# Optimization experiments

Measured on AMD Instinct MI355X. Metric: run time of the kernel, lower is better.

Reference implementation:

```python
import jax, jax.numpy as jnp
import numpy as np

B, S, D, H = 4, 2048, 256, 8
HD = D // H  # head_dim = 32
SCALING = HD ** -0.5


def setup_inputs() -> dict:
    key = jax.random.key(0)
    ks = jax.random.split(key, 10)
    glorot = jax.nn.initializers.glorot_uniform()
    inp = {
        "hidden_states": jax.random.normal(ks[0], (B, S, D), jnp.float32),
        "position_embeddings": jax.random.normal(ks[1], (B, S, D), jnp.float32),
        "attention_mask": jnp.zeros((B, S, S), jnp.float32),
        # projection params: EinsumDense 'abc,cde->abde' kernels [D, H, HD]
        "Wq": glorot(ks[2], (D, H, HD), jnp.float32),
        "bq": jnp.zeros((H, HD), jnp.float32),
        "Wk": glorot(ks[3], (D, H, HD), jnp.float32),
        "bk": jnp.zeros((H, HD), jnp.float32),
        "Wv": glorot(ks[4], (D, H, HD), jnp.float32),
        "bv": jnp.zeros((H, HD), jnp.float32),
        # out_proj: 'abc,cd->abd' kernel [D, D]
        "Wo": glorot(ks[5], (D, D), jnp.float32),
        "bo": jnp.zeros((D,), jnp.float32),
    }
    return inp


def reference(hidden_states, position_embeddings, attention_mask,
              Wq, bq, Wk, bk, Wv, bv, Wo, bo):
    # Q/K use hidden + pos embeddings; V uses original hidden states
    hp = hidden_states + position_embeddings
    q = jnp.einsum("bsd,dhe->bshe", hp, Wq) + bq            # [B,S,H,HD]
    k = jnp.einsum("bsd,dhe->bshe", hp, Wk) + bk
    v = jnp.einsum("bsd,dhe->bshe", hidden_states, Wv) + bv
    q = q * SCALING
    scores = jnp.einsum("bqhe,bkhe->bhqk", q, k)            # [B,H,S,S]
    scores = scores + attention_mask[:, None, :, :]         # additive mask
    attn = jax.nn.softmax(scores, axis=-1)
    ctx = jnp.einsum("bhqk,bkhe->bqhe", attn, v)            # [B,S,H,HD]
    ctx = ctx.reshape(ctx.shape[0], ctx.shape[1], D)        # [B,S,D]
    out = jnp.einsum("bsd,de->bse", ctx, Wo) + bo
    return out
```

## Files before the change

kernel.cpp:

```cpp
#include <hip/hip_runtime.h>
#include <hip/hip_bf16.h>

#define Bsz 4
#define Ssz 2048
#define Dsz 256
#define Hh 8
#define HDd 32

typedef __attribute__((ext_vector_type(8))) short bh8;
typedef __attribute__((ext_vector_type(4))) float f4;
typedef __attribute__((ext_vector_type(4))) unsigned u4;
typedef __attribute__((ext_vector_type(2))) unsigned u2;

#define SCAL 0.17677669529663687f
#define LOG2E 1.4426950408889634f
#define QSCALE (SCAL * LOG2E)

__device__ __forceinline__ short f2bf(float f) {
    union { float f; unsigned u; } x; x.f = f;
    unsigned r = x.u + 0x7fffu + ((x.u >> 16) & 1u);
    return (short)(r >> 16);
}

__device__ __forceinline__ float bf2f(short s) {
    union { unsigned u; float f; } x;
    x.u = ((unsigned)(unsigned short)s) << 16;
    return x.f;
}

__device__ __forceinline__ float fexp2(float x) {
#if __has_builtin(__builtin_amdgcn_exp2f)
    return __builtin_amdgcn_exp2f(x);
#else
    float r; asm("v_exp_f32 %0, %1" : "=v"(r) : "v"(x)); return r;
#endif
}

__device__ __forceinline__ unsigned cvtpk(float lo, float hi) {
    unsigned r; asm("v_cvt_pk_bf16_f32 %0, %1, %2" : "=v"(r) : "v"(lo), "v"(hi));
    return r;
}

__device__ __forceinline__ void gload16(const void* g, void* l) {
    __builtin_amdgcn_global_load_lds(
        (const __attribute__((address_space(1))) unsigned int*)g,
        (__attribute__((address_space(3))) unsigned int*)l, 16, 0, 0);
}

__global__ __launch_bounds__(256) void prep_fast(
    const float* __restrict__ hid, const float* __restrict__ pos,
    const float* __restrict__ Wq, const float* __restrict__ Wk,
    const float* __restrict__ Wv, const float* __restrict__ Wo,
    const float* __restrict__ bq,
    short* __restrict__ Wf, float* __restrict__ bqs,
    short* __restrict__ hp, short* __restrict__ hv,
    int* __restrict__ flag)
{
    const int bid = blockIdx.x;
    if (bid < 256) {
        int t = bid * 256 + threadIdx.x;
        int d = t >> 8, n = t & 255;
        int off = (((d >> 5) * 16 + (n >> 4)) * 64 + ((d >> 3) & 3) * 16 + (n & 15)) * 8 + (d & 7);
        Wf[off]          = f2bf(Wq[t] * QSCALE);
        Wf[65536 + off]  = f2bf(Wk[t]);
        Wf[131072 + off] = f2bf(Wv[t]);
        Wf[196608 + off] = f2bf(Wo[t]);
        if (t == 0) *flag = 0;
        if (t < 256) bqs[t] = bq[t] * QSCALE;
    } else {
        const size_t i = ((size_t)(bid - 256) * 256 + threadIdx.x) * 8;
        f4 h1 = *(const f4*)(hid + i), h2 = *(const f4*)(hid + i + 4);
        f4 p1 = *(const f4*)(pos + i), p2 = *(const f4*)(pos + i + 4);
        union { unsigned u[4]; bh8 v; } a, b;
        a.u[0] = cvtpk(h1[0] + p1[0], h1[1] + p1[1]);
        a.u[1] = cvtpk(h1[2] + p1[2], h1[3] + p1[3]);
        a.u[2] = cvtpk(h2[0] + p2[0], h2[1] + p2[1]);
        a.u[3] = cvtpk(h2[2] + p2[2], h2[3] + p2[3]);
        b.u[0] = cvtpk(h1[0], h1[1]); b.u[1] = cvtpk(h1[2], h1[3]);
        b.u[2] = cvtpk(h2[0], h2[1]); b.u[3] = cvtpk(h2[2], h2[3]);
        *(bh8*)(hp + i) = a.v;
        *(bh8*)(hv + i) = b.v;
    }
}

__global__ __launch_bounds__(256) void qkv_scan(
    const short* __restrict__ hp, const short* __restrict__ hv,
    const short* __restrict__ Wf, const float* __restrict__ bqs,
    const float* __restrict__ bk, const float* __restrict__ bv,
    const float* __restrict__ mask, int* __restrict__ flag,
    short* __restrict__ Q, short* __restrict__ K, short* __restrict__ Vt)
{
    const int bid = blockIdx.x;
    if (bid >= 512) {
        const u4* p = (const u4*)mask + (size_t)(bid - 512) * 4096 + threadIdx.x;
        u4 v[16];
#pragma unroll
        for (int k = 0; k < 16; k++) v[k] = p[(size_t)k * 256];
        const unsigned M = 0x7fffffffu;
        u4 o = (v[0] & M) | (v[1] & M);
#pragma unroll
        for (int k = 2; k < 16; k++) o |= (v[k] & M);
        unsigned a = (o[0] | o[1]) | (o[2] | o[3]);
        if (a != 0u) atomicOr(flag, 1);
        return;
    }
    __shared__ __align__(16) char lds[16384];
    const int tid = threadIdx.x;
    const int w = tid >> 6, lane = tid & 63;
    const int lg = lane >> 4, lr = lane & 15;
    const int m0 = bid * 16;
    const int b = m0 >> 11, s0 = m0 & 2047;

    const char* hpg = (const char*)(hp + (size_t)m0 * 256);
    const char* hvg = (const char*)(hv + (size_t)m0 * 256);
    const int rsub = lr * 512 + lg * 16;
#pragma unroll
    for (int i = 0; i < 2; i++) {
        const int k0g = i * 4 + w;
        const int src = k0g * 64 + rsub;
        const int dst = k0g * 1024;
        gload16(hpg + src, lds + dst);
        gload16(hvg + src, lds + 8192 + dst);
    }
    asm volatile("s_waitcnt vmcnt(0)" ::: "memory");
    __builtin_amdgcn_s_barrier();

    const int vhalf = (s0 >> 4) & 1;
#pragma unroll
    for (int ky = 0; ky < 3; ky++) {
        const char* Al = lds + (ky < 2 ? 0 : 8192);
        const short* Wb = Wf + ky * 65536 + (w * 4) * 512 + lane * 8;
        f4 acc[4];
#pragma unroll
        for (int t = 0; t < 4; t++) acc[t] = (f4){0.f, 0.f, 0.f, 0.f};
#pragma unroll
        for (int k0g = 0; k0g < 8; k0g++) {
            bh8 af  = *(const bh8*)(Al + k0g * 1024 + lane * 16);
            bh8 bf0 = *(const bh8*)(Wb + k0g * 8192);
            bh8 bf1 = *(const bh8*)(Wb + k0g * 8192 + 512);
            bh8 bf2 = *(const bh8*)(Wb + k0g * 8192 + 1024);
            bh8 bf3 = *(const bh8*)(Wb + k0g * 8192 + 1536);
            if (ky < 2) {
                acc[0] = __builtin_amdgcn_mfma_f32_16x16x32_bf16(bf0, af, acc[0], 0, 0, 0);
                acc[1] = __builtin_amdgcn_mfma_f32_16x16x32_bf16(bf1, af, acc[1], 0, 0, 0);
                acc[2] = __builtin_amdgcn_mfma_f32_16x16x32_bf16(bf2, af, acc[2], 0, 0, 0);
                acc[3] = __builtin_amdgcn_mfma_f32_16x16x32_bf16(bf3, af, acc[3], 0, 0, 0);
            } else {
                acc[0] = __builtin_amdgcn_mfma_f32_16x16x32_bf16(af, bf0, acc[0], 0, 0, 0);
                acc[1] = __builtin_amdgcn_mfma_f32_16x16x32_bf16(af, bf1, acc[1], 0, 0, 0);
                acc[2] = __builtin_amdgcn_mfma_f32_16x16x32_bf16(af, bf2, acc[2], 0, 0, 0);
                acc[3] = __builtin_amdgcn_mfma_f32_16x16x32_bf16(af, bf3, acc[3], 0, 0, 0);
            }
        }
        if (ky < 2) {
            short* P = (ky == 0) ? Q : K;
            const float* bb = (ky == 0) ? bqs : bk;
            const int s = s0 + lr;
#pragma unroll
            for (int nt = 0; nt < 4; nt++) {
                const int nb = w * 64 + nt * 16 + lg * 4;
                const int h = nb >> 5, hd = nb & 31;
                f4 bias = *(const f4*)(bb + nb);
                u2 o = { cvtpk(acc[nt][0] + bias[0], acc[nt][1] + bias[1]),
                         cvtpk(acc[nt][2] + bias[2], acc[nt][3] + bias[3]) };
                *(u2*)(P + ((size_t)(b * Hh + h) * Ssz + s) * HDd + hd) = o;
            }
        } else {
#pragma unroll
            for (int nt = 0; nt < 4; nt++) {
                const int n = w * 64 + nt * 16 + lr;
                const int h = n >> 5, hd = n & 31;
                const float bias = bv[n];
                u2 o = { cvtpk(acc[nt][0] + bias, acc[nt][1] + bias),
                         cvtpk(acc[nt][2] + bias, acc[nt][3] + bias) };
                *(u2*)(Vt + ((size_t)(b * Hh + h) * HDd + hd) * Ssz
                           + (s0 & ~31) + lg * 8 + vhalf * 4) = o;
            }
        }
    }
}

template<int NS>
__global__ __launch_bounds__(512) void attn(
    const short* __restrict__ Q, const short* __restrict__ Kb,
    const short* __restrict__ Vt, const float* __restrict__ mask,
    const int* __restrict__ flag, short* __restrict__ ctx,
    short* __restrict__ pacc, float* __restrict__ sums)
{
    __shared__ __align__(16) char lds[24576];
    const int tid = threadIdx.x;
    const int bh = blockIdx.y, b = bh >> 3, h = bh & 7;
    const int w = tid >> 6, lane = tid & 63;
    const int lg = lane >> 4, lr = lane & 15;
    const int q0 = blockIdx.x * 128 + w * 16;
    const int kz0 = blockIdx.z * (Ssz / NS);
    constexpr int NT = Ssz / NS / 64;

    const char* Kg = (const char*)(Kb + (size_t)bh * Ssz * HDd);
    const char* Vg = (const char*)(Vt + (size_t)bh * HDd * Ssz);
    const bool um = (*flag) != 0;
    const float* mrow = mask + ((size_t)b * Ssz + q0 + lr) * Ssz;

    const char* sgp;
    size_t sstep;
    int ldo;
    if (w < 4) {
        const int kt = w * 64 + lane;
        const int kx = (kt * 16) ^ (((kt >> 3) & 3) << 4);
        sgp = Kg + (size_t)kz0 * 64 + kx;
        sstep = 4096;
        ldo = w * 1024;
    } else {
        const int vt2 = (w - 4) * 64 + lane;
        const int vrow = vt2 >> 3;
        const int vcol = ((vt2 & 7) * 16) ^ ((vrow & 7) << 4);
        sgp = Vg + (size_t)vrow * (Ssz * 2) + (size_t)kz0 * 2 + vcol;
        sstep = 128;
        ldo = 4096 + (w - 4) * 1024;
    }

    const int koff  = (lr * 64 + lg * 16) ^ (((lr >> 1) & 3) << 4);
    const int voff0 = 4096 + ((lr * 128 + lg * 16) ^ ((lr & 7) << 4));
    const int voff1 = voff0 ^ 64;

    bh8 qf = *(const bh8*)(Q + ((size_t)bh * Ssz + q0 + lr) * HDd + lg * 8);
    const f4 c8 = {-8.f, -8.f, -8.f, -8.f};
    f4 acc0 = {0.f, 0.f, 0.f, 0.f}, acc1 = {0.f, 0.f, 0.f, 0.f};
    f4 sm = {0.f, 0.f, 0.f, 0.f};
    union { unsigned u[4]; bh8 v; } ones;
#pragma unroll
    for (int j = 0; j < 4; j++) ones.u[j] = 0x3F803F80u;

    auto stage = [&](int t, int buf) {
        gload16(sgp + (size_t)t * sstep, lds + buf * 8192 + ldo);
    };

    auto compute = [&](int t, int bs) {
        const char* kp = lds + bs + koff;
        bh8 k0 = *(const bh8*)(kp);
        bh8 k1 = *(const bh8*)(kp + 1024);
        bh8 k2 = *(const bh8*)(kp + 2048);
        bh8 k3 = *(const bh8*)(kp + 3072);
        const char* vp = lds + bs;
        bh8 v00 = *(const bh8*)(vp + voff0);
        bh8 v01 = *(const bh8*)(vp + voff1);
        bh8 v10 = *(const bh8*)(vp + voff0 + 2048);
        bh8 v11 = *(const bh8*)(vp + voff1 + 2048);

        __builtin_amdgcn_s_setprio(1);
        f4 s0 = __builtin_amdgcn_mfma_f32_16x16x32_bf16(k0, qf, c8, 0, 0, 0);
        f4 s1 = __builtin_amdgcn_mfma_f32_16x16x32_bf16(k1, qf, c8, 0, 0, 0);
        f4 s2 = __builtin_amdgcn_mfma_f32_16x16x32_bf16(k2, qf, c8, 0, 0, 0);
        f4 s3 = __builtin_amdgcn_mfma_f32_16x16x32_bf16(k3, qf, c8, 0, 0, 0);
        __builtin_amdgcn_s_setprio(0);
        if (um) {
            const int kb = kz0 + t * 64;
            f4 m0v = *(const f4*)(mrow + kb + lg * 4);
            f4 m1v = *(const f4*)(mrow + kb + 16 + lg * 4);
            f4 m2v = *(const f4*)(mrow + kb + 32 + lg * 4);
            f4 m3v = *(const f4*)(mrow + kb + 48 + lg * 4);
            s0 += m0v * LOG2E; s1 += m1v * LOG2E; s2 += m2v * LOG2E; s3 += m3v * LOG2E;
        }

        float p[16];
#pragma unroll
        for (int j = 0; j < 4; j++) {
            p[j]      = fexp2(s0[j]);
            p[4 + j]  = fexp2(s1[j]);
            p[8 + j]  = fexp2(s2[j]);
            p[12 + j] = fexp2(s3[j]);
        }
        union { unsigned u[4]; bh8 v; } pf0, pf1;
        pf0.u[0] = cvtpk(p[0], p[1]);   pf0.u[1] = cvtpk(p[2], p[3]);
        pf0.u[2] = cvtpk(p[4], p[5]);   pf0.u[3] = cvtpk(p[6], p[7]);
        pf1.u[0] = cvtpk(p[8], p[9]);   pf1.u[1] = cvtpk(p[10], p[11]);
        pf1.u[2] = cvtpk(p[12], p[13]); pf1.u[3] = cvtpk(p[14], p[15]);

        __builtin_amdgcn_s_setprio(1);
        acc0 = __builtin_amdgcn_mfma_f32_16x16x32_bf16(v00, pf0.v, acc0, 0, 0, 0);
        acc0 = __builtin_amdgcn_mfma_f32_16x16x32_bf16(v01, pf1.v, acc0, 0, 0, 0);
        acc1 = __builtin_amdgcn_mfma_f32_16x16x32_bf16(v10, pf0.v, acc1, 0, 0, 0);
        acc1 = __builtin_amdgcn_mfma_f32_16x16x32_bf16(v11, pf1.v, acc1, 0, 0, 0);
        sm   = __builtin_amdgcn_mfma_f32_16x16x32_bf16(ones.v, pf0.v, sm, 0, 0, 0);
        sm   = __builtin_amdgcn_mfma_f32_16x16x32_bf16(ones.v, pf1.v, sm, 0, 0, 0);
        __builtin_amdgcn_s_setprio(0);
    };

    stage(0, 0);
    stage(1, 1);
    for (int t = 0; t < NT - 1; ++t) {
        asm volatile("s_waitcnt vmcnt(1)" ::: "memory");
        __builtin_amdgcn_s_barrier();
        if (t + 2 < NT) stage(t + 2, (t + 2) % 3);
        compute(t, (t % 3) * 8192);
    }
    asm volatile("s_waitcnt vmcnt(0)" ::: "memory");
    __builtin_amdgcn_s_barrier();
    compute(NT - 1, ((NT - 1) % 3) * 8192);

    const float sum = sm[0];

    if constexpr (NS == 1) {
        float inv = 1.f / sum;
        short* cp = ctx + ((size_t)(b * Ssz + q0 + lr)) * Dsz + h * HDd + lg * 4;
#pragma unroll
        for (int r = 0; r < 4; r++) {
            cp[r]      = f2bf(acc0[r] * inv);
            cp[16 + r] = f2bf(acc1[r] * inv);
        }
    } else {
        const size_t rbase = ((size_t)blockIdx.z * (Bsz * Hh) + bh) * Ssz + q0 + lr;
        short* pa = pacc + rbase * HDd;
        *(u2*)(pa + lg * 4)      = (u2){cvtpk(acc0[0], acc0[1]), cvtpk(acc0[2], acc0[3])};
        *(u2*)(pa + 16 + lg * 4) = (u2){cvtpk(acc1[0], acc1[1]), cvtpk(acc1[2], acc1[3])};
        if (lg == 0) sums[rbase] = sum;
    }
}

template<int SPLIT>
__global__ __launch_bounds__(256) void out_gemm(
    const short* __restrict__ ctx, const short* __restrict__ pacc,
    const float* __restrict__ sums, const short* __restrict__ WfO,
    const float* __restrict__ bo, float* __restrict__ out)
{
    const int w = threadIdx.x >> 6, lane = threadIdx.x & 63;
    const int lg = lane >> 4, lr = lane & 15;
    const int m0 = blockIdx.x * 16;
    const int row = m0 + lr;
    const int b = row >> 11, q = row & 2047;
    f4 acc[4];
#pragma unroll
    for (int t = 0; t < 4; t++) acc[t] = (f4){0.f, 0.f, 0.f, 0.f};
    const short* ap = ctx + (size_t)row * 256 + lg * 8;
    const short* Wb = WfO + (w * 4) * 512 + lane * 8;
    constexpr size_t R = (size_t)(Bsz * Hh) * Ssz;
#pragma unroll
    for (int k0g = 0; k0g < 8; k0g++) {
        union { unsigned u[4]; bh8 v; } af;
        if constexpr (SPLIT) {
            const int h = k0g;
            const size_t pr = ((size_t)(b * Hh + h)) * Ssz + q;
            const float inv = 1.f / (sums[pr] + sums[R + pr]);
            bh8 x0 = *(const bh8*)(pacc + pr * HDd + lg * 8);
            bh8 x1 = *(const bh8*)(pacc + (R + pr) * HDd + lg * 8);
            af.u[0] = cvtpk((bf2f(x0[0]) + bf2f(x1[0])) * inv, (bf2f(x0[1]) + bf2f(x1[1])) * inv);
            af.u[1] = cvtpk((bf2f(x0[2]) + bf2f(x1[2])) * inv, (bf2f(x0[3]) + bf2f(x1[3])) * inv);
            af.u[2] = cvtpk((bf2f(x0[4]) + bf2f(x1[4])) * inv, (bf2f(x0[5]) + bf2f(x1[5])) * inv);
            af.u[3] = cvtpk((bf2f(x0[6]) + bf2f(x1[6])) * inv, (bf2f(x0[7]) + bf2f(x1[7])) * inv);
        } else {
            af.v = *(const bh8*)(ap + k0g * 32);
        }
#pragma unroll
        for (int nt = 0; nt < 4; nt++) {
            bh8 bf = *(const bh8*)(Wb + k0g * 8192 + nt * 512);
            acc[nt] = __builtin_amdgcn_mfma_f32_16x16x32_bf16(bf, af.v, acc[nt], 0, 0, 0);
        }
    }
#pragma unroll
    for (int nt = 0; nt < 4; nt++) {
        const int nb = w * 64 + nt * 16 + lg * 4;
        f4 bias = *(const f4*)(bo + nb);
        f4 res = acc[nt] + bias;
        *(f4*)(out + (size_t)row * 256 + nb) = res;
    }
}

extern "C" void kernel_launch(void* const* d_in, const int* in_sizes, int n_in,
                              void* d_out, int out_size, void* d_ws, size_t ws_size,
                              hipStream_t stream)
{
    const float* hid  = (const float*)d_in[0];
    const float* pos  = (const float*)d_in[1];
    const float* mask = (const float*)d_in[2];
    const float* Wq   = (const float*)d_in[3];
    const float* bq   = (const float*)d_in[4];
    const float* Wk   = (const float*)d_in[5];
    const float* bk   = (const float*)d_in[6];
    const float* Wv   = (const float*)d_in[7];
    const float* bv   = (const float*)d_in[8];
    const float* Wo   = (const float*)d_in[9];
    const float* bo   = (const float*)d_in[10];
    float* out = (float*)d_out;

    char* ws = (char*)d_ws;
    short* Wf   = (short*)(ws);
    float* bqs  = (float*)(ws + (512 << 10));
    int*   flag = (int*)  (ws + (516 << 10));
    short* hp   = (short*)(ws + (1  << 20));
    short* hv   = (short*)(ws + (5  << 20));
    short* Qb   = (short*)(ws + (9  << 20));
    short* Kb   = (short*)(ws + (13 << 20));
    short* Vtb  = (short*)(ws + (17 << 20));
    short* ctxb = (short*)(ws + (21 << 20));
    short* pacc = (short*)(ws + (25 << 20));
    float* sums = (float*)(ws + (34 << 20));

    prep_fast<<<1280, 256, 0, stream>>>(hid, pos, Wq, Wk, Wv, Wo, bq, Wf, bqs, hp, hv, flag);
    qkv_scan<<<1536, 256, 0, stream>>>(hp, hv, Wf, bqs, bk, bv, mask, flag, Qb, Kb, Vtb);

    const bool split = ws_size >= ((size_t)36 << 20);
    if (split) {
        attn<2><<<dim3(16, 32, 2), 512, 0, stream>>>(Qb, Kb, Vtb, mask, flag, ctxb, pacc, sums);
        out_gemm<1><<<512, 256, 0, stream>>>(ctxb, pacc, sums, Wf + 196608, bo, out);
    } else {
        attn<1><<<dim3(16, 32, 1), 512, 0, stream>>>(Qb, Kb, Vtb, mask, flag, ctxb, pacc, sums);
        out_gemm<0><<<512, 256, 0, stream>>>(ctxb, pacc, sums, Wf + 196608, bo, out);
    }
}
```

Baseline: 65.91 us.

## Double query rows per attention wave and fuse input conversion into QKV projection

The attention kernel now has each wave process 32 query rows instead of 16, so every K/V fragment loaded from LDS feeds twice as many MFMAs. The grid is halved to match and the launch bounds gain an occupancy hint. Separately, the fp32-to-bf16 conversion of hidden+pos and hidden is moved out of the prep kernel into the QKV kernel's LDS staging, which removes the intermediate hp/hv round trip through global memory. In exchange, attention uses more registers per wave and runs fewer blocks, and the QKV kernel now waits on synchronous fp32 global loads.

New measurement: 64.39 us. -2.3%, faster.

```diff
diff --git a/kernel.cpp b/kernel.cpp
--- a/kernel.cpp
+++ b/kernel.cpp
@@ -48,43 +48,25 @@
 }
 
 __global__ __launch_bounds__(256) void prep_fast(
-    const float* __restrict__ hid, const float* __restrict__ pos,
     const float* __restrict__ Wq, const float* __restrict__ Wk,
     const float* __restrict__ Wv, const float* __restrict__ Wo,
     const float* __restrict__ bq,
     short* __restrict__ Wf, float* __restrict__ bqs,
-    short* __restrict__ hp, short* __restrict__ hv,
     int* __restrict__ flag)
 {
-    const int bid = blockIdx.x;
-    if (bid < 256) {
-        int t = bid * 256 + threadIdx.x;
-        int d = t >> 8, n = t & 255;
-        int off = (((d >> 5) * 16 + (n >> 4)) * 64 + ((d >> 3) & 3) * 16 + (n & 15)) * 8 + (d & 7);
-        Wf[off]          = f2bf(Wq[t] * QSCALE);
-        Wf[65536 + off]  = f2bf(Wk[t]);
-        Wf[131072 + off] = f2bf(Wv[t]);
-        Wf[196608 + off] = f2bf(Wo[t]);
-        if (t == 0) *flag = 0;
-        if (t < 256) bqs[t] = bq[t] * QSCALE;
-    } else {
-        const size_t i = ((size_t)(bid - 256) * 256 + threadIdx.x) * 8;
-        f4 h1 = *(const f4*)(hid + i), h2 = *(const f4*)(hid + i + 4);
-        f4 p1 = *(const f4*)(pos + i), p2 = *(const f4*)(pos + i + 4);
-        union { unsigned u[4]; bh8 v; } a, b;
-        a.u[0] = cvtpk(h1[0] + p1[0], h1[1] + p1[1]);
-        a.u[1] = cvtpk(h1[2] + p1[2], h1[3] + p1[3]);
-        a.u[2] = cvtpk(h2[0] + p2[0], h2[1] + p2[1]);
-        a.u[3] = cvtpk(h2[2] + p2[2], h2[3] + p2[3]);
-        b.u[0] = cvtpk(h1[0], h1[1]); b.u[1] = cvtpk(h1[2], h1[3]);
-        b.u[2] = cvtpk(h2[0], h2[1]); b.u[3] = cvtpk(h2[2], h2[3]);
-        *(bh8*)(hp + i) = a.v;
-        *(bh8*)(hv + i) = b.v;
-    }
+    int t = blockIdx.x * 256 + threadIdx.x;
+    int d = t >> 8, n = t & 255;
+    int off = (((d >> 5) * 16 + (n >> 4)) * 64 + ((d >> 3) & 3) * 16 + (n & 15)) * 8 + (d & 7);
+    Wf[off]          = f2bf(Wq[t] * QSCALE);
+    Wf[65536 + off]  = f2bf(Wk[t]);
+    Wf[131072 + off] = f2bf(Wv[t]);
+    Wf[196608 + off] = f2bf(Wo[t]);
+    if (t == 0) *flag = 0;
+    if (t < 256) bqs[t] = bq[t] * QSCALE;
 }
 
 __global__ __launch_bounds__(256) void qkv_scan(
-    const short* __restrict__ hp, const short* __restrict__ hv,
+    const float* __restrict__ hid, const float* __restrict__ pos,
     const short* __restrict__ Wf, const float* __restrict__ bqs,
     const float* __restrict__ bk, const float* __restrict__ bv,
     const float* __restrict__ mask, int* __restrict__ flag,
@@ -111,18 +93,28 @@
     const int m0 = bid * 16;
     const int b = m0 >> 11, s0 = m0 & 2047;
 
-    const char* hpg = (const char*)(hp + (size_t)m0 * 256);
-    const char* hvg = (const char*)(hv + (size_t)m0 * 256);
-    const int rsub = lr * 512 + lg * 16;
-#pragma unroll
-    for (int i = 0; i < 2; i++) {
-        const int k0g = i * 4 + w;
-        const int src = k0g * 64 + rsub;
-        const int dst = k0g * 1024;
-        gload16(hpg + src, lds + dst);
-        gload16(hvg + src, lds + 8192 + dst);
-    }
-    asm volatile("s_waitcnt vmcnt(0)" ::: "memory");
+    {
+        const int row = tid >> 4, c = tid & 15;
+        const float* hb = hid + (size_t)(m0 + row) * 256 + c * 16;
+        const float* pb = pos + (size_t)(m0 + row) * 256 + c * 16;
+        f4 h0 = *(const f4*)(hb), h1 = *(const f4*)(hb + 4);
+        f4 h2 = *(const f4*)(hb + 8), h3 = *(const f4*)(hb + 12);
+        f4 p0 = *(const f4*)(pb), p1 = *(const f4*)(pb + 4);
+        f4 p2 = *(const f4*)(pb + 8), p3 = *(const f4*)(pb + 12);
+        const int off = ((c >> 1) * 1024) + (((2 * c) & 3) * 256) + row * 16;
+        u4 hp0 = { cvtpk(h0[0] + p0[0], h0[1] + p0[1]), cvtpk(h0[2] + p0[2], h0[3] + p0[3]),
+                   cvtpk(h1[0] + p1[0], h1[1] + p1[1]), cvtpk(h1[2] + p1[2], h1[3] + p1[3]) };
+        u4 hp1 = { cvtpk(h2[0] + p2[0], h2[1] + p2[1]), cvtpk(h2[2] + p2[2], h2[3] + p2[3]),
+                   cvtpk(h3[0] + p3[0], h3[1] + p3[1]), cvtpk(h3[2] + p3[2], h3[3] + p3[3]) };
+        u4 hv0 = { cvtpk(h0[0], h0[1]), cvtpk(h0[2], h0[3]),
+                   cvtpk(h1[0], h1[1]), cvtpk(h1[2], h1[3]) };
+        u4 hv1 = { cvtpk(h2[0], h2[1]), cvtpk(h2[2], h2[3]),
+                   cvtpk(h3[0], h3[1]), cvtpk(h3[2], h3[3]) };
+        *(u4*)(lds + off)          = hp0;
+        *(u4*)(lds + off + 256)    = hp1;
+        *(u4*)(lds + 8192 + off)       = hv0;
+        *(u4*)(lds + 8192 + off + 256) = hv1;
+    }
     __builtin_amdgcn_s_barrier();
 
     const int vhalf = (s0 >> 4) & 1;
@@ -181,7 +173,7 @@
 }
 
 template<int NS>
-__global__ __launch_bounds__(512) void attn(
+__global__ __launch_bounds__(512, 4) void attn(
     const short* __restrict__ Q, const short* __restrict__ Kb,
     const short* __restrict__ Vt, const float* __restrict__ mask,
     const int* __restrict__ flag, short* __restrict__ ctx,
@@ -192,14 +184,15 @@
     const int bh = blockIdx.y, b = bh >> 3, h = bh & 7;
     const int w = tid >> 6, lane = tid & 63;
     const int lg = lane >> 4, lr = lane & 15;
-    const int q0 = blockIdx.x * 128 + w * 16;
+    const int q0 = blockIdx.x * 256 + w * 32;
     const int kz0 = blockIdx.z * (Ssz / NS);
     constexpr int NT = Ssz / NS / 64;
 
     const char* Kg = (const char*)(Kb + (size_t)bh * Ssz * HDd);
     const char* Vg = (const char*)(Vt + (size_t)bh * HDd * Ssz);
     const bool um = (*flag) != 0;
-    const float* mrow = mask + ((size_t)b * Ssz + q0 + lr) * Ssz;
+    const float* mrow0 = mask + ((size_t)b * Ssz + q0 + lr) * Ssz;
+    const float* mrow1 = mrow0 + (size_t)16 * Ssz;
 
     const char* sgp;
     size_t sstep;
@@ -223,10 +216,12 @@
     const int voff0 = 4096 + ((lr * 128 + lg * 16) ^ ((lr & 7) << 4));
     const int voff1 = voff0 ^ 64;
 
-    bh8 qf = *(const bh8*)(Q + ((size_t)bh * Ssz + q0 + lr) * HDd + lg * 8);
+    const short* Qw = Q + ((size_t)bh * Ssz + q0) * HDd;
+    bh8 qf0 = *(const bh8*)(Qw + (size_t)lr * HDd + lg * 8);
+    bh8 qf1 = *(const bh8*)(Qw + (size_t)(16 + lr) * HDd + lg * 8);
     const f4 c8 = {-8.f, -8.f, -8.f, -8.f};
-    f4 acc0 = {0.f, 0.f, 0.f, 0.f}, acc1 = {0.f, 0.f, 0.f, 0.f};
-    f4 sm = {0.f, 0.f, 0.f, 0.f};
+    f4 a00 = {0.f,0.f,0.f,0.f}, a01 = a00, a10 = a00, a11 = a00;
+    f4 sm0 = a00, sm1 = a00;
     union { unsigned u[4]; bh8 v; } ones;
 #pragma unroll
     for (int j = 0; j < 4; j++) ones.u[j] = 0x3F803F80u;
@@ -248,41 +243,66 @@
         bh8 v11 = *(const bh8*)(vp + voff1 + 2048);
 
         __builtin_amdgcn_s_setprio(1);
-        f4 s0 = __builtin_amdgcn_mfma_f32_16x16x32_bf16(k0, qf, c8, 0, 0, 0);
-        f4 s1 = __builtin_amdgcn_mfma_f32_16x16x32_bf16(k1, qf, c8, 0, 0, 0);
-        f4 s2 = __builtin_amdgcn_mfma_f32_16x16x32_bf16(k2, qf, c8, 0, 0, 0);
-        f4 s3 = __builtin_amdgcn_mfma_f32_16x16x32_bf16(k3, qf, c8, 0, 0, 0);
+        f4 s00 = __builtin_amdgcn_mfma_f32_16x16x32_bf16(k0, qf0, c8, 0, 0, 0);
+        f4 s01 = __builtin_amdgcn_mfma_f32_16x16x32_bf16(k1, qf0, c8, 0, 0, 0);
+        f4 s02 = __builtin_amdgcn_mfma_f32_16x16x32_bf16(k2, qf0, c8, 0, 0, 0);
+        f4 s03 = __builtin_amdgcn_mfma_f32_16x16x32_bf16(k3, qf0, c8, 0, 0, 0);
+        f4 s10 = __builtin_amdgcn_mfma_f32_16x16x32_bf16(k0, qf1, c8, 0, 0, 0);
+        f4 s11 = __builtin_amdgcn_mfma_f32_16x16x32_bf16(k1, qf1, c8, 0, 0, 0);
+        f4 s12 = __builtin_amdgcn_mfma_f32_16x16x32_bf16(k2, qf1, c8, 0, 0, 0);
+        f4 s13 = __builtin_amdgcn_mfma_f32_16x16x32_bf16(k3, qf1, c8, 0, 0, 0);
         __builtin_amdgcn_s_setprio(0);
         if (um) {
             const int kb = kz0 + t * 64;
-            f4 m0v = *(const f4*)(mrow + kb + lg * 4);
-            f4 m1v = *(const f4*)(mrow + kb + 16 + lg * 4);
-            f4 m2v = *(const f4*)(mrow + kb + 32 + lg * 4);
-            f4 m3v = *(const f4*)(mrow + kb + 48 + lg * 4);
-            s0 += m0v * LOG2E; s1 += m1v * LOG2E; s2 += m2v * LOG2E; s3 += m3v * LOG2E;
-        }
-
-        float p[16];
-#pragma unroll
-        for (int j = 0; j < 4; j++) {
-            p[j]      = fexp2(s0[j]);
-            p[4 + j]  = fexp2(s1[j]);
-            p[8 + j]  = fexp2(s2[j]);
-            p[12 + j] = fexp2(s3[j]);
-        }
-        union { unsigned u[4]; bh8 v; } pf0, pf1;
-        pf0.u[0] = cvtpk(p[0], p[1]);   pf0.u[1] = cvtpk(p[2], p[3]);
-        pf0.u[2] = cvtpk(p[4], p[5]);   pf0.u[3] = cvtpk(p[6], p[7]);
-        pf1.u[0] = cvtpk(p[8], p[9]);   pf1.u[1] = cvtpk(p[10], p[11]);
-        pf1.u[2] = cvtpk(p[12], p[13]); pf1.u[3] = cvtpk(p[14], p[15]);
+            s00 += *(const f4*)(mrow0 + kb + lg * 4) * LOG2E;
+            s01 += *(const f4*)(mrow0 + kb + 16 + lg * 4) * LOG2E;
+            s02 += *(const f4*)(mrow0 + kb + 32 + lg * 4) * LOG2E;
+            s03 += *(const f4*)(mrow0 + kb + 48 + lg * 4) * LOG2E;
+            s10 += *(const f4*)(mrow1 + kb + lg * 4) * LOG2E;
+            s11 += *(const f4*)(mrow1 + kb + 16 + lg * 4) * LOG2E;
+            s12 += *(const f4*)(mrow1 + kb + 32 + lg * 4) * LOG2E;
+            s13 += *(const f4*)(mrow1 + kb + 48 + lg * 4) * LOG2E;
+        }
+
+        union { unsigned u[4]; bh8 v; } pf00, pf01, pf10, pf11;
+        {
+            float p[16];
+#pragma unroll
+            for (int j = 0; j < 4; j++) {
+                p[j] = fexp2(s00[j]); p[4+j] = fexp2(s01[j]);
+                p[8+j] = fexp2(s02[j]); p[12+j] = fexp2(s03[j]);
+            }
+            pf00.u[0] = cvtpk(p[0], p[1]);   pf00.u[1] = cvtpk(p[2], p[3]);
+            pf00.u[2] = cvtpk(p[4], p[5]);   pf00.u[3] = cvtpk(p[6], p[7]);
+            pf01.u[0] = cvtpk(p[8], p[9]);   pf01.u[1] = cvtpk(p[10], p[11]);
+            pf01.u[2] = cvtpk(p[12], p[13]); pf01.u[3] = cvtpk(p[14], p[15]);
+        }
+        {
+            float p[16];
+#pragma unroll
+            for (int j = 0; j < 4; j++) {
+                p[j] = fexp2(s10[j]); p[4+j] = fexp2(s11[j]);
+                p[8+j] = fexp2(s12[j]); p[12+j] = fexp2(s13[j]);
+            }
+            pf10.u[0] = cvtpk(p[0], p[1]);   pf10.u[1] = cvtpk(p[2], p[3]);
+            pf10.u[2] = cvtpk(p[4], p[5]);   pf10.u[3] = cvtpk(p[6], p[7]);
+            pf11.u[0] = cvtpk(p[8], p[9]);   pf11.u[1] = cvtpk(p[10], p[11]);
+            pf11.u[2] = cvtpk(p[12], p[13]); pf11.u[3] = cvtpk(p[14], p[15]);
+        }
 
         __builtin_amdgcn_s_setprio(1);
-        acc0 = __builtin_amdgcn_mfma_f32_16x16x32_bf16(v00, pf0.v, acc0, 0, 0, 0);
-        acc0 = __builtin_amdgcn_mfma_f32_16x16x32_bf16(v01, pf1.v, acc0, 0, 0, 0);
-        acc1 = __builtin_amdgcn_mfma_f32_16x16x32_bf16(v10, pf0.v, acc1, 0, 0, 0);
-        acc1 = __builtin_amdgcn_mfma_f32_16x16x32_bf16(v11, pf1.v, acc1, 0, 0, 0);
-        sm   = __builtin_amdgcn_mfma_f32_16x16x32_bf16(ones.v, pf0.v, sm, 0, 0, 0);
-        sm   = __builtin_amdgcn_mfma_f32_16x16x32_bf16(ones.v, pf1.v, sm, 0, 0, 0);
+        a00 = __builtin_amdgcn_mfma_f32_16x16x32_bf16(v00, pf00.v, a00, 0, 0, 0);
+        a00 = __builtin_amdgcn_mfma_f32_16x16x32_bf16(v01, pf01.v, a00, 0, 0, 0);
+        a01 = __builtin_amdgcn_mfma_f32_16x16x32_bf16(v10, pf00.v, a01, 0, 0, 0);
+        a01 = __builtin_amdgcn_mfma_f32_16x16x32_bf16(v11, pf01.v, a01, 0, 0, 0);
+        sm0 = __builtin_amdgcn_mfma_f32_16x16x32_bf16(ones.v, pf00.v, sm0, 0, 0, 0);
+        sm0 = __builtin_amdgcn_mfma_f32_16x16x32_bf16(ones.v, pf01.v, sm0, 0, 0, 0);
+        a10 = __builtin_amdgcn_mfma_f32_16x16x32_bf16(v00, pf10.v, a10, 0, 0, 0);
+        a10 = __builtin_amdgcn_mfma_f32_16x16x32_bf16(v01, pf11.v, a10, 0, 0, 0);
+        a11 = __builtin_amdgcn_mfma_f32_16x16x32_bf16(v10, pf10.v, a11, 0, 0, 0);
+        a11 = __builtin_amdgcn_mfma_f32_16x16x32_bf16(v11, pf11.v, a11, 0, 0, 0);
+        sm1 = __builtin_amdgcn_mfma_f32_16x16x32_bf16(ones.v, pf10.v, sm1, 0, 0, 0);
+        sm1 = __builtin_amdgcn_mfma_f32_16x16x32_bf16(ones.v, pf11.v, sm1, 0, 0, 0);
         __builtin_amdgcn_s_setprio(0);
     };
 
@@ -298,22 +318,31 @@
     __builtin_amdgcn_s_barrier();
     compute(NT - 1, ((NT - 1) % 3) * 8192);
 
-    const float sum = sm[0];
+    const float sum0 = sm0[0], sum1 = sm1[0];
 
     if constexpr (NS == 1) {
-        float inv = 1.f / sum;
-        short* cp = ctx + ((size_t)(b * Ssz + q0 + lr)) * Dsz + h * HDd + lg * 4;
+        float inv0 = 1.f / sum0, inv1 = 1.f / sum1;
+        short* cp0 = ctx + ((size_t)(b * Ssz + q0 + lr)) * Dsz + h * HDd + lg * 4;
+        short* cp1 = cp0 + (size_t)16 * Dsz;
 #pragma unroll
         for (int r = 0; r < 4; r++) {
-            cp[r]      = f2bf(acc0[r] * inv);
-            cp[16 + r] = f2bf(acc1[r] * inv);
+            cp0[r]      = f2bf(a00[r] * inv0);
+            cp0[16 + r] = f2bf(a01[r] * inv0);
+            cp1[r]      = f2bf(a10[r] * inv1);
+            cp1[16 + r] = f2bf(a11[r] * inv1);
         }
     } else {
         const size_t rbase = ((size_t)blockIdx.z * (Bsz * Hh) + bh) * Ssz + q0 + lr;
-        short* pa = pacc + rbase * HDd;
-        *(u2*)(pa + lg * 4)      = (u2){cvtpk(acc0[0], acc0[1]), cvtpk(acc0[2], acc0[3])};
-        *(u2*)(pa + 16 + lg * 4) = (u2){cvtpk(acc1[0], acc1[1]), cvtpk(acc1[2], acc1[3])};
-        if (lg == 0) sums[rbase] = sum;
+        short* pa0 = pacc + rbase * HDd;
+        short* pa1 = pa0 + (size_t)16 * HDd;
+        *(u2*)(pa0 + lg * 4)      = (u2){cvtpk(a00[0], a00[1]), cvtpk(a00[2], a00[3])};
+        *(u2*)(pa0 + 16 + lg * 4) = (u2){cvtpk(a01[0], a01[1]), cvtpk(a01[2], a01[3])};
+        *(u2*)(pa1 + lg * 4)      = (u2){cvtpk(a10[0], a10[1]), cvtpk(a10[2], a10[3])};
+        *(u2*)(pa1 + 16 + lg * 4) = (u2){cvtpk(a11[0], a11[1]), cvtpk(a11[2], a11[3])};
+        if (lg == 0) {
+            sums[rbase]      = sum0;
+            sums[rbase + 16] = sum1;
+        }
     }
 }
 
@@ -386,8 +415,6 @@
     short* Wf   = (short*)(ws);
     float* bqs  = (float*)(ws + (512 << 10));
     int*   flag = (int*)  (ws + (516 << 10));
-    short* hp   = (short*)(ws + (1  << 20));
-    short* hv   = (short*)(ws + (5  << 20));
     short* Qb   = (short*)(ws + (9  << 20));
     short* Kb   = (short*)(ws + (13 << 20));
     short* Vtb  = (short*)(ws + (17 << 20));
@@ -395,15 +422,15 @@
     short* pacc = (short*)(ws + (25 << 20));
     float* sums = (float*)(ws + (34 << 20));
 
-    prep_fast<<<1280, 256, 0, stream>>>(hid, pos, Wq, Wk, Wv, Wo, bq, Wf, bqs, hp, hv, flag);
-    qkv_scan<<<1536, 256, 0, stream>>>(hp, hv, Wf, bqs, bk, bv, mask, flag, Qb, Kb, Vtb);
+    prep_fast<<<256, 256, 0, stream>>>(Wq, Wk, Wv, Wo, bq, Wf, bqs, flag);
+    qkv_scan<<<1536, 256, 0, stream>>>(hid, pos, Wf, bqs, bk, bv, mask, flag, Qb, Kb, Vtb);
 
     const bool split = ws_size >= ((size_t)36 << 20);
     if (split) {
-        attn<2><<<dim3(16, 32, 2), 512, 0, stream>>>(Qb, Kb, Vtb, mask, flag, ctxb, pacc, sums);
+        attn<2><<<dim3(8, 32, 2), 512, 0, stream>>>(Qb, Kb, Vtb, mask, flag, ctxb, pacc, sums);
         out_gemm<1><<<512, 256, 0, stream>>>(ctxb, pacc, sums, Wf + 196608, bo, out);
     } else {
-        attn<1><<<dim3(16, 32, 1), 512, 0, stream>>>(Qb, Kb, Vtb, mask, flag, ctxb, pacc, sums);
+        attn<1><<<dim3(8, 32, 1), 512, 0, stream>>>(Qb, Kb, Vtb, mask, flag, ctxb, pacc, sums);
         out_gemm<0><<<512, 256, 0, stream>>>(ctxb, pacc, sums, Wf + 196608, bo, out);
     }
 }
```
